# Optimization experiments

Hardware: AMD Instinct MI355X
Metric: run time of the kernel (lower is better)

Reference implementation:

```python
import jax, jax.numpy as jnp
import numpy as np

B, S, V, D, P, H, L = 8, 512, 256, 1024, 128, 8, 4


def setup_inputs() -> dict:
    key = jax.random.key(0)
    ks = jax.random.split(key, 8)
    tokens = jax.random.normal(ks[0], (B, S, V), dtype=jnp.float32)
    # causal additive mask (0 on/below diagonal, -1e9 above)
    att_mask = jnp.where(jnp.tril(jnp.ones((S, S), dtype=bool)), 0.0, -1e9).astype(jnp.float32)
    embed_W = jax.random.normal(ks[1], (V, D), dtype=jnp.float32) * 0.02
    unembed_W = jax.random.normal(ks[2], (D, V), dtype=jnp.float32) * 0.02
    wq = jax.random.normal(ks[3], (L, H, D, P), dtype=jnp.float32) * 0.02
    wk = jax.random.normal(ks[4], (L, H, D, P), dtype=jnp.float32) * 0.02
    wv = jax.random.normal(ks[5], (L, H, D, P), dtype=jnp.float32) * 0.02
    wo = jax.random.normal(ks[6], (L, H, P, D), dtype=jnp.float32) * 0.02
    return {"tokens": tokens, "att_mask": att_mask, "embed_W": embed_W,
            "unembed_W": unembed_W, "wq": wq, "wk": wk, "wv": wv, "wo": wo}


def reference(tokens, att_mask, embed_W, unembed_W, wq, wk, wv, wo):
    scale = jnp.asarray(P, tokens.dtype) ** 0.5
    stream = jnp.einsum('bsv,vd->bsd', tokens, embed_W)  # embed
    streams = [stream]
    atts = []
    for l in range(L):  # loop over layers (structural); heads are batched
        q = jnp.einsum('bsd,hdp->bhsp', stream, wq[l])
        k = jnp.einsum('bsd,hdp->bhsp', stream, wk[l])
        v = jnp.einsum('bsd,hdp->bhsp', stream, wv[l])
        logit = jnp.einsum('bhqp,bhkp->bhqk', q, k) / scale + att_mask
        att = jax.nn.softmax(logit, axis=-1)            # [B,H,S,S]
        comb = jnp.einsum('bhqk,bhkp->bhqp', att, v)
        delta = jnp.einsum('bhsp,hpd->bsd', comb, wo[l])  # sum over heads
        stream = stream + delta
        streams.append(stream)
        atts.append(att)
    logits = jnp.einsum('bsd,dv->bsv', stream, unembed_W)
    return (logits, jnp.stack(atts), jnp.stack(streams))
```

## Files before the change

### kernel.cpp

```cpp
#include <hip/hip_runtime.h>
#include <math.h>

typedef __bf16 bf16x8 __attribute__((ext_vector_type(8)));
typedef float  f32x4  __attribute__((ext_vector_type(4)));
typedef _Float16 f16x4 __attribute__((ext_vector_type(4)));

#define GLOAD16(g, l) __builtin_amdgcn_global_load_lds( \
    (const __attribute__((address_space(1))) void*)(g), \
    (__attribute__((address_space(3))) void*)(l), 16, 0, 0)

__global__ __launch_bounds__(256) void cvt_bf16(const float* __restrict__ in,
                                                __bf16* __restrict__ out)
{
    const int i = (blockIdx.x * 256 + threadIdx.x) * 4;
    float4 f = *(const float4*)(in + i);
    out[i + 0] = (__bf16)f.x; out[i + 1] = (__bf16)f.y;
    out[i + 2] = (__bf16)f.z; out[i + 3] = (__bf16)f.w;
}

__global__ __launch_bounds__(256) void transpose_cvt(
    const float* __restrict__ in, __bf16* __restrict__ out,
    int C, int outLd, long inZ, int zdiv, long outZ1, long outZ2)
{
    __shared__ float t[32][33];
    const int z = blockIdx.z, z1 = z / zdiv, z2 = z % zdiv;
    in  += (long)z * inZ;
    out += z1 * outZ1 + z2 * outZ2;
    const int c0 = blockIdx.x * 32, r0 = blockIdx.y * 32;
    const int tx = threadIdx.x, ty = threadIdx.y;
    #pragma unroll
    for (int i = 0; i < 32; i += 8)
        t[ty + i][tx] = in[(long)(r0 + ty + i) * C + c0 + tx];
    __syncthreads();
    #pragma unroll
    for (int i = 0; i < 32; i += 8)
        out[(long)(c0 + ty + i) * outLd + r0 + tx] = (__bf16)t[tx][ty + i];
}

__global__ __launch_bounds__(256) void mfma_gemm(
    const __bf16* __restrict__ A, const __bf16* __restrict__ Bt,
    int lda, int ldb, int K,
    float* __restrict__ outF, int ldf,
    __bf16* __restrict__ outB, int ldo,
    __bf16* __restrict__ vt,
    const float* __restrict__ resid, int ldr)
{
    __shared__ __bf16 As[128 * 32];
    __shared__ __bf16 Bs[128 * 32];

    const int m0 = blockIdx.y * 128, n0 = blockIdx.x * 128;
    const int t = threadIdx.x, w = t >> 6, ln = t & 63;
    const int r = ln & 15, q = ln >> 4;
    const int wm = (w >> 1) * 64, wn = (w & 1) * 64;

    f32x4 acc[4][4];
    #pragma unroll
    for (int i = 0; i < 4; ++i)
        #pragma unroll
        for (int j = 0; j < 4; ++j)
            acc[i][j] = f32x4{0.f, 0.f, 0.f, 0.f};

    const int srow = ln >> 2, scol = (ln & 3) * 8;

    for (int k0 = 0; k0 < K; k0 += 32) {
        #pragma unroll
        for (int c = 0; c < 2; ++c) {
            const int ch = w + c * 4;
            const __bf16* ga = A  + (long)(m0 + ch * 16 + srow) * lda + k0 + scol;
            GLOAD16(ga, &As[ch * 512]);
            const __bf16* gb = Bt + (long)(n0 + ch * 16 + srow) * ldb + k0 + scol;
            GLOAD16(gb, &Bs[ch * 512]);
        }
        __syncthreads();
        bf16x8 af[4], bv[4];
        #pragma unroll
        for (int i = 0; i < 4; ++i) af[i] = *(const bf16x8*)&As[(wm + i * 16 + r) * 32 + q * 8];
        #pragma unroll
        for (int i = 0; i < 4; ++i) bv[i] = *(const bf16x8*)&Bs[(wn + i * 16 + r) * 32 + q * 8];
        #pragma unroll
        for (int i = 0; i < 4; ++i)
            #pragma unroll
            for (int j = 0; j < 4; ++j)
                acc[i][j] = __builtin_amdgcn_mfma_f32_16x16x32_bf16(af[i], bv[j], acc[i][j], 0, 0, 0);
        __syncthreads();
    }

    #pragma unroll
    for (int i = 0; i < 4; ++i) {
        #pragma unroll
        for (int j = 0; j < 4; ++j) {
            #pragma unroll
            for (int g = 0; g < 4; ++g) {
                const int m = m0 + wm + i * 16 + q * 4 + g;
                const int n = n0 + wn + j * 16 + r;
                float v = acc[i][j][g];
                if (resid) v += resid[(long)m * ldr + n];
                if (outF)  outF[(long)m * ldf + n] = v;
                if (outB) {
                    if (vt && n >= 2048) {
                        const int p = n - 2048, h = p >> 7, pp = p & 127;
                        const int b = m >> 9, s = m & 511;
                        vt[(((long)(b * 8 + h)) * 128 + pp) * 512 + s] = (__bf16)v;
                    } else {
                        outB[(long)m * ldo + n] = (__bf16)v;
                    }
                }
            }
        }
    }
}

__global__ __launch_bounds__(256, 3) void flash2(
    const __bf16* __restrict__ QK, const __bf16* __restrict__ Vt,
    float* __restrict__ atts, __bf16* __restrict__ comb)
{
    const int f = blockIdx.x;
    const int bh = (f & 7) * 8 + ((f >> 3) & 7);
    const int qt = f >> 6;
    const int b = bh >> 3, h = bh & 7;
    const int nkt = (qt >> 1) + 1;
    const float rs = 0.08838834764831845f;

    __shared__ __bf16 KVs[128 * 136];
    __shared__ __bf16 Ps[4 * 16 * 136];

    const int t = threadIdx.x, w = t >> 6, ln = t & 63;
    const int r = ln & 15, q = ln >> 4;

    const long qrow = (long)(b * 512 + qt * 64 + w * 16 + r);
    bf16x8 Qf[4];
    #pragma unroll
    for (int kp = 0; kp < 4; ++kp)
        Qf[kp] = *(const bf16x8*)(QK + qrow * 2048 + h * 128 + kp * 32 + q * 8);

    f16x4 E16[4][8];
    float L[4] = {0.f, 0.f, 0.f, 0.f};

    #pragma unroll
    for (int kt = 0; kt < 4; ++kt) {
        if (kt < nkt) {
            __syncthreads();
            const __bf16* ksrc = QK + ((long)(b * 512 + kt * 128)) * 2048 + 1024 + h * 128;
            #pragma unroll
            for (int c0 = 0; c0 < 8; ++c0) {
                const int c = c0 * 256 + t;
                const int row = c >> 4, col = (c & 15) * 8;
                *(bf16x8*)&KVs[row * 136 + col] = *(const bf16x8*)(ksrc + (long)row * 2048 + col);
            }
            __syncthreads();

            #pragma unroll
            for (int nb = 0; nb < 8; ++nb) {
                f32x4 s = f32x4{0.f, 0.f, 0.f, 0.f};
                #pragma unroll
                for (int kp = 0; kp < 4; ++kp) {
                    bf16x8 bv = *(const bf16x8*)&KVs[(nb * 16 + r) * 136 + kp * 32 + q * 8];
                    s = __builtin_amdgcn_mfma_f32_16x16x32_bf16(Qf[kp], bv, s, 0, 0, 0);
                }
                const int kc = kt * 128 + nb * 16 + r;
                f16x4 e;
                #pragma unroll
                for (int g = 0; g < 4; ++g) {
                    float ev = __expf(s[g] * rs - 3.0f);
                    if (kt == nkt - 1) {
                        const int qr = qt * 64 + w * 16 + q * 4 + g;
                        if (kc > qr) ev = 0.f;
                    }
                    L[g] += ev;
                    e[g] = (_Float16)ev;
                }
                E16[kt][nb] = e;
            }
        }
    }

    float linv[4];
    #pragma unroll
    for (int g = 0; g < 4; ++g) {
        float Lg = L[g];
        #pragma unroll
        for (int s = 1; s < 16; s <<= 1) Lg += __shfl_xor(Lg, s);
        linv[g] = 1.0f / Lg;
    }

    f32x4 O[8];
    #pragma unroll
    for (int pb = 0; pb < 8; ++pb) O[pb] = f32x4{0.f, 0.f, 0.f, 0.f};

    float* abase = atts + (long)bh * 262144 + (long)(qt * 64 + w * 16) * 512;
    __bf16* psw = &Ps[w * 16 * 136];

    #pragma unroll
    for (int kt = 0; kt < 4; ++kt) {
        if (kt < nkt) {
            __syncthreads();
            const __bf16* vsrc = Vt + (long)bh * 65536 + kt * 128;
            #pragma unroll
            for (int c0 = 0; c0 < 8; ++c0) {
                const int c = c0 * 256 + t;
                const int row = c >> 4, col = (c & 15) * 8;
                *(bf16x8*)&KVs[row * 136 + col] = *(const bf16x8*)(vsrc + (long)row * 512 + col);
            }
            __syncthreads();

            #pragma unroll
            for (int nb = 0; nb < 8; ++nb) {
                f16x4 e = E16[kt][nb];
                #pragma unroll
                for (int g = 0; g < 4; ++g) {
                    float p = (float)e[g] * linv[g];
                    abase[(long)(q * 4 + g) * 512 + kt * 128 + nb * 16 + r] = p;
                    psw[(q * 4 + g) * 136 + nb * 16 + r] = (__bf16)p;
                }
            }
            bf16x8 Pf[4];
            #pragma unroll
            for (int kp = 0; kp < 4; ++kp)
                Pf[kp] = *(const bf16x8*)&psw[r * 136 + kp * 32 + q * 8];
            #pragma unroll
            for (int pb = 0; pb < 8; ++pb) {
                #pragma unroll
                for (int kp = 0; kp < 4; ++kp) {
                    bf16x8 bv = *(const bf16x8*)&KVs[(pb * 16 + r) * 136 + kp * 32 + q * 8];
                    O[pb] = __builtin_amdgcn_mfma_f32_16x16x32_bf16(Pf[kp], bv, O[pb], 0, 0, 0);
                }
            }
        }
    }

    {
        float* zbase = atts + (long)bh * 262144 + (long)(qt * 64) * 512;
        float4 z4 = {0.f, 0.f, 0.f, 0.f};
        for (int ktz = nkt; ktz < 4; ++ktz) {
            #pragma unroll
            for (int c0 = 0; c0 < 8; ++c0) {
                const int c = c0 * 256 + t;
                const int row = c >> 5, col = (c & 31) * 4;
                *(float4*)&zbase[(long)row * 512 + ktz * 128 + col] = z4;
            }
        }
    }

    const long crow = (long)(b * 512 + qt * 64 + w * 16);
    #pragma unroll
    for (int pb = 0; pb < 8; ++pb)
        #pragma unroll
        for (int g = 0; g < 4; ++g)
            comb[(crow + q * 4 + g) * 1024 + h * 128 + pb * 16 + r] = (__bf16)O[pb][g];
}

extern "C" void kernel_launch(void* const* d_in, const int* in_sizes, int n_in,
                              void* d_out, int out_size, void* d_ws, size_t ws_size,
                              hipStream_t stream)
{
    const float* tokens = (const float*)d_in[0];
    const float* embedW = (const float*)d_in[2];
    const float* unembW = (const float*)d_in[3];
    const float* wq     = (const float*)d_in[4];
    const float* wk     = (const float*)d_in[5];
    const float* wv     = (const float*)d_in[6];
    const float* wo     = (const float*)d_in[7];

    float* out       = (float*)d_out;
    float* logits_o  = out;
    float* atts_o    = out + 1048576L;
    float* streams_o = atts_o + 67108864L;

    __bf16* embedWt   = (__bf16*)d_ws;
    __bf16* unembWt   = embedWt + 262144;
    __bf16* WtAll     = unembWt + 262144;
    __bf16* WotAll    = WtAll + 12582912;
    __bf16* tokens_bf = WotAll + 4194304;
    __bf16* stream_bf = tokens_bf + 1048576;
    __bf16* QKbuf     = stream_bf + 4194304;
    __bf16* Vt        = QKbuf + 8388608;
    __bf16* comb      = Vt + 4194304;

    const dim3 T(32, 8), G1(256);

    cvt_bf16<<<dim3(1024), G1, 0, stream>>>(tokens, tokens_bf);
    transpose_cvt<<<dim3(32, 8, 1), T, 0, stream>>>(embedW, embedWt, 1024, 256, 0, 1, 0, 0);
    transpose_cvt<<<dim3(8, 32, 1), T, 0, stream>>>(unembW, unembWt, 256, 1024, 0, 1, 0, 0);
    transpose_cvt<<<dim3(4, 32, 32), T, 0, stream>>>(wq, WtAll,           128, 1024, 131072, 8, 3145728, 131072);
    transpose_cvt<<<dim3(4, 32, 32), T, 0, stream>>>(wk, WtAll + 1048576, 128, 1024, 131072, 8, 3145728, 131072);
    transpose_cvt<<<dim3(4, 32, 32), T, 0, stream>>>(wv, WtAll + 2097152, 128, 1024, 131072, 8, 3145728, 131072);
    transpose_cvt<<<dim3(32, 32, 4), T, 0, stream>>>(wo, WotAll, 1024, 1024, 1048576, 1, 1048576, 0);

    mfma_gemm<<<dim3(8, 32), G1, 0, stream>>>(
        tokens_bf, embedWt, 256, 256, 256,
        streams_o, 1024, stream_bf, 1024, nullptr, nullptr, 0);

    for (int l = 0; l < 4; ++l) {
        float* st  = streams_o + (long)l * 4194304;
        float* stn = st + 4194304;
        float* attl = atts_o + (long)l * 16777216;

        mfma_gemm<<<dim3(24, 32), G1, 0, stream>>>(
            stream_bf, WtAll + (long)l * 3145728, 1024, 1024, 1024,
            nullptr, 0, QKbuf, 2048, Vt, nullptr, 0);

        flash2<<<dim3(512), G1, 0, stream>>>(QKbuf, Vt, attl, comb);

        mfma_gemm<<<dim3(8, 32), G1, 0, stream>>>(
            comb, WotAll + (long)l * 1048576, 1024, 1024, 1024,
            stn, 1024, stream_bf, 1024, nullptr, st, 1024);
    }

    mfma_gemm<<<dim3(2, 32), G1, 0, stream>>>(
        stream_bf, unembWt, 1024, 1024, 1024,
        logits_o, 256, nullptr, 0, nullptr, nullptr, 0);
}
```

Before: 883.5 us.

## Transpose flash MFMA operands, vectorize attention stores, remap GEMM blocks, fuse QKV transposes

The flash kernel swaps the MFMA operand order so each lane holds one query row and four consecutive keys. This lets attention probabilities, the P tile and comb be written with float4/bf16x4 vector stores, and the row-sum reduction shrinks to two shuffles. Query tiles now run in reverse order so the heavier causal tiles start first, and the flash occupancy hint drops from 3 to 2 blocks per SM. The GEMM remaps block IDs in an interleaved order, intended to improve L2 locality. The three QKV weight transposes are merged into one launch to cut launch overhead.

```diff
diff --git a/kernel.cpp b/kernel.cpp
--- a/kernel.cpp
+++ b/kernel.cpp
@@ -2,6 +2,7 @@
 #include <math.h>
 
 typedef __bf16 bf16x8 __attribute__((ext_vector_type(8)));
+typedef __bf16 bf16x4 __attribute__((ext_vector_type(4)));
 typedef float  f32x4  __attribute__((ext_vector_type(4)));
 typedef _Float16 f16x4 __attribute__((ext_vector_type(4)));
 
@@ -35,6 +36,27 @@
     #pragma unroll
     for (int i = 0; i < 32; i += 8)
         out[(long)(c0 + ty + i) * outLd + r0 + tx] = (__bf16)t[tx][ty + i];
+}
+
+__global__ __launch_bounds__(256) void transpose_qkv(
+    const float* __restrict__ wq, const float* __restrict__ wk,
+    const float* __restrict__ wv, __bf16* __restrict__ out)
+{
+    __shared__ float tl[32][33];
+    const int z = blockIdx.z;
+    const int m = z >> 5, zz = z & 31;
+    const float* in = (m == 0 ? wq : m == 1 ? wk : wv) + (long)zz * 131072;
+    __bf16* o = out + (long)m * 1048576 + (long)(zz >> 3) * 3145728
+                    + (long)(zz & 7) * 131072;
+    const int c0 = blockIdx.x * 32, r0 = blockIdx.y * 32;
+    const int tx = threadIdx.x, ty = threadIdx.y;
+    #pragma unroll
+    for (int i = 0; i < 32; i += 8)
+        tl[ty + i][tx] = in[(long)(r0 + ty + i) * 128 + c0 + tx];
+    __syncthreads();
+    #pragma unroll
+    for (int i = 0; i < 32; i += 8)
+        o[(long)(c0 + ty + i) * 1024 + r0 + tx] = (__bf16)tl[tx][ty + i];
 }
 
 __global__ __launch_bounds__(256) void mfma_gemm(
@@ -48,7 +70,11 @@
     __shared__ __bf16 As[128 * 32];
     __shared__ __bf16 Bs[128 * 32];
 
-    const int m0 = blockIdx.y * 128, n0 = blockIdx.x * 128;
+    int lid = blockIdx.y * gridDim.x + blockIdx.x;
+    const int nwg = gridDim.x * gridDim.y;
+    lid = (lid & 7) * (nwg >> 3) + (lid >> 3);
+    const int m0 = (lid / gridDim.x) * 128, n0 = (lid % gridDim.x) * 128;
+
     const int t = threadIdx.x, w = t >> 6, ln = t & 63;
     const int r = ln & 15, q = ln >> 4;
     const int wm = (w >> 1) * 64, wn = (w & 1) * 64;
@@ -110,13 +136,13 @@
     }
 }
 
-__global__ __launch_bounds__(256, 3) void flash2(
+__global__ __launch_bounds__(256, 2) void flash2(
     const __bf16* __restrict__ QK, const __bf16* __restrict__ Vt,
     float* __restrict__ atts, __bf16* __restrict__ comb)
 {
     const int f = blockIdx.x;
     const int bh = (f & 7) * 8 + ((f >> 3) & 7);
-    const int qt = f >> 6;
+    const int qt = 7 - (f >> 6);
     const int b = bh >> 3, h = bh & 7;
     const int nkt = (qt >> 1) + 1;
     const float rs = 0.08838834764831845f;
@@ -134,7 +160,8 @@
         Qf[kp] = *(const bf16x8*)(QK + qrow * 2048 + h * 128 + kp * 32 + q * 8);
 
     f16x4 E16[4][8];
-    float L[4] = {0.f, 0.f, 0.f, 0.f};
+    float Lsum = 0.f;
+    const int qr = qt * 64 + w * 16 + r;
 
     #pragma unroll
     for (int kt = 0; kt < 4; ++kt) {
@@ -154,19 +181,16 @@
                 f32x4 s = f32x4{0.f, 0.f, 0.f, 0.f};
                 #pragma unroll
                 for (int kp = 0; kp < 4; ++kp) {
-                    bf16x8 bv = *(const bf16x8*)&KVs[(nb * 16 + r) * 136 + kp * 32 + q * 8];
-                    s = __builtin_amdgcn_mfma_f32_16x16x32_bf16(Qf[kp], bv, s, 0, 0, 0);
-                }
-                const int kc = kt * 128 + nb * 16 + r;
+                    bf16x8 av = *(const bf16x8*)&KVs[(nb * 16 + r) * 136 + kp * 32 + q * 8];
+                    s = __builtin_amdgcn_mfma_f32_16x16x32_bf16(av, Qf[kp], s, 0, 0, 0);
+                }
                 f16x4 e;
                 #pragma unroll
                 for (int g = 0; g < 4; ++g) {
                     float ev = __expf(s[g] * rs - 3.0f);
-                    if (kt == nkt - 1) {
-                        const int qr = qt * 64 + w * 16 + q * 4 + g;
-                        if (kc > qr) ev = 0.f;
-                    }
-                    L[g] += ev;
+                    const int kc = kt * 128 + nb * 16 + q * 4 + g;
+                    if (kt == nkt - 1 && kc > qr) ev = 0.f;
+                    Lsum += ev;
                     e[g] = (_Float16)ev;
                 }
                 E16[kt][nb] = e;
@@ -174,20 +198,15 @@
         }
     }
 
-    float linv[4];
-    #pragma unroll
-    for (int g = 0; g < 4; ++g) {
-        float Lg = L[g];
-        #pragma unroll
-        for (int s = 1; s < 16; s <<= 1) Lg += __shfl_xor(Lg, s);
-        linv[g] = 1.0f / Lg;
-    }
+    Lsum += __shfl_xor(Lsum, 16);
+    Lsum += __shfl_xor(Lsum, 32);
+    const float linv = 1.0f / Lsum;
 
     f32x4 O[8];
     #pragma unroll
     for (int pb = 0; pb < 8; ++pb) O[pb] = f32x4{0.f, 0.f, 0.f, 0.f};
 
-    float* abase = atts + (long)bh * 262144 + (long)(qt * 64 + w * 16) * 512;
+    float* arow = atts + (long)bh * 262144 + (long)qr * 512;
     __bf16* psw = &Ps[w * 16 * 136];
 
     #pragma unroll
@@ -206,12 +225,16 @@
             #pragma unroll
             for (int nb = 0; nb < 8; ++nb) {
                 f16x4 e = E16[kt][nb];
+                float4 pf4;
+                bf16x4 pb4;
                 #pragma unroll
                 for (int g = 0; g < 4; ++g) {
-                    float p = (float)e[g] * linv[g];
-                    abase[(long)(q * 4 + g) * 512 + kt * 128 + nb * 16 + r] = p;
-                    psw[(q * 4 + g) * 136 + nb * 16 + r] = (__bf16)p;
-                }
+                    float p = (float)e[g] * linv;
+                    (&pf4.x)[g] = p;
+                    pb4[g] = (__bf16)p;
+                }
+                *(float4*)&arow[kt * 128 + nb * 16 + q * 4] = pf4;
+                *(bf16x4*)&psw[r * 136 + nb * 16 + q * 4] = pb4;
             }
             bf16x8 Pf[4];
             #pragma unroll
@@ -221,8 +244,8 @@
             for (int pb = 0; pb < 8; ++pb) {
                 #pragma unroll
                 for (int kp = 0; kp < 4; ++kp) {
-                    bf16x8 bv = *(const bf16x8*)&KVs[(pb * 16 + r) * 136 + kp * 32 + q * 8];
-                    O[pb] = __builtin_amdgcn_mfma_f32_16x16x32_bf16(Pf[kp], bv, O[pb], 0, 0, 0);
+                    bf16x8 vv = *(const bf16x8*)&KVs[(pb * 16 + r) * 136 + kp * 32 + q * 8];
+                    O[pb] = __builtin_amdgcn_mfma_f32_16x16x32_bf16(vv, Pf[kp], O[pb], 0, 0, 0);
                 }
             }
         }
@@ -241,12 +264,13 @@
         }
     }
 
-    const long crow = (long)(b * 512 + qt * 64 + w * 16);
-    #pragma unroll
-    for (int pb = 0; pb < 8; ++pb)
-        #pragma unroll
-        for (int g = 0; g < 4; ++g)
-            comb[(crow + q * 4 + g) * 1024 + h * 128 + pb * 16 + r] = (__bf16)O[pb][g];
+    #pragma unroll
+    for (int pb = 0; pb < 8; ++pb) {
+        bf16x4 ob;
+        #pragma unroll
+        for (int g = 0; g < 4; ++g) ob[g] = (__bf16)O[pb][g];
+        *(bf16x4*)&comb[qrow * 1024 + h * 128 + pb * 16 + q * 4] = ob;
+    }
 }
 
 extern "C" void kernel_launch(void* const* d_in, const int* in_sizes, int n_in,
@@ -281,9 +305,7 @@
     cvt_bf16<<<dim3(1024), G1, 0, stream>>>(tokens, tokens_bf);
     transpose_cvt<<<dim3(32, 8, 1), T, 0, stream>>>(embedW, embedWt, 1024, 256, 0, 1, 0, 0);
     transpose_cvt<<<dim3(8, 32, 1), T, 0, stream>>>(unembW, unembWt, 256, 1024, 0, 1, 0, 0);
-    transpose_cvt<<<dim3(4, 32, 32), T, 0, stream>>>(wq, WtAll,           128, 1024, 131072, 8, 3145728, 131072);
-    transpose_cvt<<<dim3(4, 32, 32), T, 0, stream>>>(wk, WtAll + 1048576, 128, 1024, 131072, 8, 3145728, 131072);
-    transpose_cvt<<<dim3(4, 32, 32), T, 0, stream>>>(wv, WtAll + 2097152, 128, 1024, 131072, 8, 3145728, 131072);
+    transpose_qkv<<<dim3(4, 32, 96), T, 0, stream>>>(wq, wk, wv, WtAll);
     transpose_cvt<<<dim3(32, 32, 4), T, 0, stream>>>(wo, WotAll, 1024, 1024, 1048576, 1, 1048576, 0);
 
     mfma_gemm<<<dim3(8, 32), G1, 0, stream>>>(
```

Result: no change. 876.6 us (-0.8%).
